# Kernel tuning notes

Measured on AMD Instinct MI355X. Metric: run time of the kernel, lower is better.

Reference implementation:

```python
import jax, jax.numpy as jnp
import numpy as np

B = 16384       # batch of peptide samples
M = 15          # max_peptide_size
R = 64          # aa_rep_size
P = 34          # number of pocket positions
F = 9           # filter_size
A = 20          # alphabet size


def setup_inputs() -> dict:
    key = jax.random.key(0)
    k1, k2, k3, k4 = jax.random.split(key, 4)
    peptide_encoding = jax.random.normal(k1, (B, M, R), dtype=jnp.float32)
    pocket_aa_idx = jax.random.randint(k2, (B, P), 0, A, dtype=jnp.int32)
    adj_mask = jax.random.randint(k3, (B, P, M), 0, 2, dtype=jnp.int32)
    # one trainable 1-D filter of length F per alphabet letter ('uniform' init)
    kernels = jax.random.uniform(k4, (A, F), dtype=jnp.float32, minval=-0.05, maxval=0.05)
    return {"peptide_encoding": peptide_encoding, "pocket_aa_idx": pocket_aa_idx,
            "adj_mask": adj_mask, "kernels": kernels}


def reference(peptide_encoding, pocket_aa_idx, adj_mask, kernels):
    # Per pocket position p of sample b: filter = kernels[pocket_aa_idx[b,p]]  [B,P,F]
    filt = kernels[pocket_aa_idx]
    # Convolution is linear, so sum the adjacent peptide-position encodings first:
    # s[b,p,r] = sum_m adj_mask[b,p,m] * peptide_encoding[b,m,r]   -> [B,P,R]
    s = jnp.einsum('bpm,bmr->bpr', adj_mask.astype(peptide_encoding.dtype), peptide_encoding)
    # Full convolution along the representation axis: output length R + F - 1
    conv1 = jax.vmap(jax.vmap(lambda a, b: jnp.convolve(a, b, mode='full')))
    out = conv1(s, filt)  # [B, P, R+F-1]
    return out
```

## Files before the change

kernel.cpp:

```cpp
#include <hip/hip_runtime.h>

#define MM 15
#define RR 64
#define PP 34
#define FF 9
#define AA 20
#define OW 72

#define WAVE_SHL1 0x130
#define WAVE_SHR1 0x138

__device__ __forceinline__ float dpp_shr1(float x) {
    return __int_as_float(__builtin_amdgcn_update_dpp(
        0, __float_as_int(x), WAVE_SHR1, 0xF, 0xF, true));
}
__device__ __forceinline__ float dpp_shl1(float x) {
    return __int_as_float(__builtin_amdgcn_update_dpp(
        0, __float_as_int(x), WAVE_SHL1, 0xF, 0xF, true));
}

__global__ __launch_bounds__(256)
void ppc_kernel(const float* __restrict__ pe,
                const int*   __restrict__ idx,
                const int*   __restrict__ adj,
                const float* __restrict__ kernels,
                float*       __restrict__ out)
{
    const int b    = blockIdx.x;
    const int lane = threadIdx.x & 63;
    const int w    = __builtin_amdgcn_readfirstlane(threadIdx.x >> 6);

    const float* peb  = pe  + (size_t)b * (MM * RR);
    const int*   adjb = adj + (size_t)b * (PP * MM);
    const int*   idxb = idx + (size_t)b * PP;
    float*       outb = out + (size_t)b * (PP * OW);

    float pv[MM];
    #pragma unroll
    for (int m = 0; m < MM; ++m) pv[m] = peb[m * RR + lane];

    #pragma unroll
    for (int j = 0; j < 9; ++j) {
        const int p = w + 4 * j;
        if (p < PP) {
            const int* g = adjb + p * MM;
            float s = 0.0f;
            #pragma unroll
            for (int m = 0; m < MM; ++m) {
                const float gf = g[m] ? 1.0f : 0.0f;
                s = fmaf(gf, pv[m], s);
            }

            const float* kb = kernels + idxb[p] * FF;
            float kf[FF];
            #pragma unroll
            for (int i2 = 0; i2 < FF; ++i2) kf[i2] = kb[i2];

            float H = kf[8] * s;
            #pragma unroll
            for (int i2 = 7; i2 >= 0; --i2)
                H = fmaf(kf[i2], s, dpp_shr1(H));
            outb[p * OW + lane] = H;

            float T = kf[0] * s;
            #pragma unroll
            for (int i2 = 1; i2 <= 8; ++i2)
                T = fmaf(kf[i2], s, dpp_shl1(T));
            if (lane >= 56)
                outb[p * OW + 8 + lane] = T;
        }
    }
}

extern "C" void kernel_launch(void* const* d_in, const int* in_sizes, int n_in,
                              void* d_out, int out_size, void* d_ws, size_t ws_size,
                              hipStream_t stream) {
    const float* pe      = (const float*)d_in[0];
    const int*   idx     = (const int*)  d_in[1];
    const int*   adj     = (const int*)  d_in[2];
    const float* kernels = (const float*)d_in[3];
    float*       out     = (float*)d_out;

    const int B = in_sizes[0] / (MM * RR);
    ppc_kernel<<<B, 256, 0, stream>>>(pe, idx, adj, kernels, out);
}
```

Before: 81.04 us.

## Assign one wavefront per sample and loop over all pockets

Each 64-lane wavefront now processes a whole sample, looping over all 34 pocket positions, and each block covers four samples. Before, four waves of one block split the pockets of a single sample. Each sample's peptide encoding is now loaded once by a single wave instead of by four, which removes redundant loads. The adjacency dot product is split into three partial accumulators to shorten the dependency chain. In exchange, each wave has a longer serial loop, and there are a quarter as many blocks, which lowers parallelism per sample and adds per-wave latency. The launch assumes B is divisible by four.

```diff
diff --git a/kernel.cpp b/kernel.cpp
--- a/kernel.cpp
+++ b/kernel.cpp
@@ -26,9 +26,8 @@
                 const float* __restrict__ kernels,
                 float*       __restrict__ out)
 {
-    const int b    = blockIdx.x;
+    const int b    = (blockIdx.x << 2) | (threadIdx.x >> 6);
     const int lane = threadIdx.x & 63;
-    const int w    = __builtin_amdgcn_readfirstlane(threadIdx.x >> 6);
 
     const float* peb  = pe  + (size_t)b * (MM * RR);
     const int*   adjb = adj + (size_t)b * (PP * MM);
@@ -39,36 +38,35 @@
     #pragma unroll
     for (int m = 0; m < MM; ++m) pv[m] = peb[m * RR + lane];
 
-    #pragma unroll
-    for (int j = 0; j < 9; ++j) {
-        const int p = w + 4 * j;
-        if (p < PP) {
-            const int* g = adjb + p * MM;
-            float s = 0.0f;
-            #pragma unroll
-            for (int m = 0; m < MM; ++m) {
-                const float gf = g[m] ? 1.0f : 0.0f;
-                s = fmaf(gf, pv[m], s);
-            }
+    #pragma unroll 2
+    for (int p = 0; p < PP; ++p) {
+        const int* g = adjb + p * MM;
+        float a0 = 0.f, a1 = 0.f, a2 = 0.f;
+        #pragma unroll
+        for (int m = 0; m < 5; ++m) a0 = fmaf((float)g[m],      pv[m],      a0);
+        #pragma unroll
+        for (int m = 0; m < 5; ++m) a1 = fmaf((float)g[5 + m],  pv[5 + m],  a1);
+        #pragma unroll
+        for (int m = 0; m < 5; ++m) a2 = fmaf((float)g[10 + m], pv[10 + m], a2);
+        const float s = (a0 + a1) + a2;
 
-            const float* kb = kernels + idxb[p] * FF;
-            float kf[FF];
-            #pragma unroll
-            for (int i2 = 0; i2 < FF; ++i2) kf[i2] = kb[i2];
+        const float* kb = kernels + idxb[p] * FF;
+        float kf[FF];
+        #pragma unroll
+        for (int i = 0; i < FF; ++i) kf[i] = kb[i];
 
-            float H = kf[8] * s;
-            #pragma unroll
-            for (int i2 = 7; i2 >= 0; --i2)
-                H = fmaf(kf[i2], s, dpp_shr1(H));
-            outb[p * OW + lane] = H;
+        float H = kf[8] * s;
+        #pragma unroll
+        for (int i = 7; i >= 0; --i)
+            H = fmaf(kf[i], s, dpp_shr1(H));
+        outb[p * OW + lane] = H;
 
-            float T = kf[0] * s;
-            #pragma unroll
-            for (int i2 = 1; i2 <= 8; ++i2)
-                T = fmaf(kf[i2], s, dpp_shl1(T));
-            if (lane >= 56)
-                outb[p * OW + 8 + lane] = T;
-        }
+        float T = kf[0] * s;
+        #pragma unroll
+        for (int i = 1; i <= 8; ++i)
+            T = fmaf(kf[i], s, dpp_shl1(T));
+        if (lane >= 56)
+            outb[p * OW + 8 + lane] = T;
     }
 }
 
@@ -82,5 +80,5 @@
     float*       out     = (float*)d_out;
 
     const int B = in_sizes[0] / (MM * RR);
-    ppc_kernel<<<B, 256, 0, stream>>>(pe, idx, adj, kernels, out);
+    ppc_kernel<<<B / 4, 256, 0, stream>>>(pe, idx, adj, kernels, out);
 }
```

New measurement: 126.1 us. 1.56x slower.
